# Kernel tuning notes

Hardware: AMD Instinct MI355X
Metric: run time of the kernel (lower is better)

The kernel has to match this reference:

```python
import jax, jax.numpy as jnp
import numpy as np

B, C, H, W = 2, 192, 256, 256
HEADS = 6


def _conv1x1(x, w, b):
    # x: [b,ci,h,w], w: [co,ci,1,1], b: [co]
    return jnp.einsum('oi,bihw->bohw', w[:, :, 0, 0], x) + b[None, :, None, None]


def _dwconv3x3(x, w, b):
    # depthwise 3x3, padding=1; x: [b,c,h,w], w: [c,1,3,3], b: [c]
    y = jax.lax.conv_general_dilated(
        x, w, window_strides=(1, 1), padding='SAME',
        feature_group_count=x.shape[1],
        dimension_numbers=('NCHW', 'OIHW', 'NCHW'))
    return y + b[None, :, None, None]


def _l2norm(t, eps=1e-12):
    # F.normalize(dim=-1): x / max(||x||_2, eps)
    n = jnp.sqrt(jnp.sum(t * t, axis=-1, keepdims=True))
    return t / jnp.maximum(n, eps)


def setup_inputs() -> dict:
    key = jax.random.key(0)
    ks = jax.random.split(key, 12)
    s = 0.02
    return {
        'feat_guide': jax.random.normal(ks[0], (B, C, H, W), jnp.float32),
        'feat_op': jax.random.normal(ks[1], (B, C, H, W), jnp.float32),
        'q_w': jax.random.normal(ks[2], (C, C, 1, 1), jnp.float32) * s,
        'q_b': jax.random.normal(ks[3], (C,), jnp.float32) * s,
        'kv_w': jax.random.normal(ks[4], (2 * C, C, 1, 1), jnp.float32) * s,
        'kv_b': jax.random.normal(ks[5], (2 * C,), jnp.float32) * s,
        'q_dw_w': jax.random.normal(ks[6], (C, 1, 3, 3), jnp.float32) * s,
        'q_dw_b': jax.random.normal(ks[7], (C,), jnp.float32) * s,
        'kv_dw_w': jax.random.normal(ks[8], (2 * C, 1, 3, 3), jnp.float32) * s,
        'kv_dw_b': jax.random.normal(ks[9], (2 * C,), jnp.float32) * s,
        'proj_w': jax.random.normal(ks[10], (C, C, 1, 1), jnp.float32) * s,
        'proj_b': jax.random.normal(ks[11], (C,), jnp.float32) * s,
        'temperature': jnp.ones((HEADS, 1, 1), jnp.float32),
    }


def reference(feat_guide, feat_op, q_w, q_b, kv_w, kv_b, q_dw_w, q_dw_b,
              kv_dw_w, kv_dw_b, proj_w, proj_b, temperature):
    b, c, h, w = feat_guide.shape
    q = _dwconv3x3(_conv1x1(feat_guide, q_w, q_b), q_dw_w, q_dw_b)
    kv = _dwconv3x3(_conv1x1(feat_op, kv_w, kv_b), kv_dw_w, kv_dw_b)
    k, v = jnp.split(kv, 2, axis=1)

    def heads(t):  # [b,c,h,w] -> [b,heads,c/heads,hw]
        return t.reshape(b, HEADS, c // HEADS, h * w)

    q = _l2norm(heads(q))
    k = _l2norm(heads(k))
    v = heads(v)
    # channel-wise attention: [b,heads,c',c'] scores over hw
    attn = jnp.einsum('bhcn,bhdn->bhcd', q, k) * temperature[None]
    attn = jax.nn.softmax(attn, axis=-1)
    out = jnp.einsum('bhcd,bhdn->bhcn', attn, v).reshape(b, c, h, w)
    return _conv1x1(out, proj_w, proj_b)
```

## Files before the change

kernel.cpp:

```cpp
#include <hip/hip_runtime.h>

#define HW_N 65536
#define CC 192
#define NCHUNKS 128

typedef __attribute__((ext_vector_type(8))) short short8v;
typedef __attribute__((ext_vector_type(4))) short short4v;
typedef __attribute__((ext_vector_type(4))) float f32x4;

__device__ __forceinline__ float bf2f(unsigned short u) {
  union { unsigned int i; float f; } v; v.i = ((unsigned int)u) << 16; return v.f;
}
__device__ __forceinline__ unsigned short f2bf(float f) {
  union { float f; unsigned int i; } v; v.f = f;
  unsigned int r = v.i + 0x7fffu + ((v.i >> 16) & 1u);
  return (unsigned short)(r >> 16);
}

__global__ __launch_bounds__(256) void cvt_w(
    const float* __restrict__ qw, const float* __restrict__ kvw,
    unsigned short* __restrict__ Wq, unsigned short* __restrict__ Wkv) {
  const int i = (blockIdx.x * 256 + threadIdx.x) * 8;
  const float* src; unsigned short* dst; int off;
  if (i < 36864) { src = qw; dst = Wq; off = i; }
  else { src = kvw; dst = Wkv; off = i - 36864; }
  unsigned short tmp[8];
#pragma unroll
  for (int j = 0; j < 8; ++j) tmp[j] = f2bf(src[off + j]);
  *(short8v*)(dst + off) = *(short8v*)tmp;
}

template <int INF32, int OUTF32, int PERB>
__global__ __launch_bounds__(512) void conv_gemm(
    const void* __restrict__ X_, const unsigned short* __restrict__ W,
    const float* __restrict__ bias, void* __restrict__ out_,
    int Mtot, int msplit) {
  __shared__ unsigned short Bt[2][128][40];
  __shared__ unsigned short Rp[96][144];
  const int d = blockIdx.x;
  int mt, nt;
  if (msplit == 2) { mt = (d >> 3) & 1; nt = (d & 7) | ((d >> 4) << 3); }
  else { mt = 0; nt = d; }
  const int m0 = mt * 192, n0 = nt * 128;
  const int b = blockIdx.z;
  const int t = threadIdx.x;
  const int lane = t & 63, wv = t >> 6;
  const int l15 = lane & 15, lg = lane >> 4;
  const int wm = wv & 3, wn = wv >> 2;
  const int mrow = m0 + wm * 48;
  const int nw = wn * 64;
  const int nq = t & 31;
  const int kp = t >> 5;
  const size_t xb = (size_t)b * CC * (size_t)HW_N + n0 + nq * 4;
  const unsigned short* Wb = W + (PERB ? (size_t)b * Mtot * CC : 0);

  unsigned int pk[4];
  auto gload = [&](int kc) {
    const size_t xo = xb + (size_t)(kc * 32 + kp * 2) * (size_t)HW_N;
    if (INF32) {
      f32x4 v0 = *(const f32x4*)((const float*)X_ + xo);
      f32x4 v1 = *(const f32x4*)((const float*)X_ + xo + HW_N);
#pragma unroll
      for (int j = 0; j < 4; ++j)
        pk[j] = (unsigned int)f2bf(v0[j]) | ((unsigned int)f2bf(v1[j]) << 16);
    } else {
      short4v a0 = *(const short4v*)((const unsigned short*)X_ + xo);
      short4v a1 = *(const short4v*)((const unsigned short*)X_ + xo + HW_N);
#pragma unroll
      for (int j = 0; j < 4; ++j)
        pk[j] = (unsigned int)(unsigned short)a0[j] | ((unsigned int)(unsigned short)a1[j] << 16);
    }
  };
  auto lwrite = [&](int buf) {
#pragma unroll
    for (int j = 0; j < 4; ++j)
      *(unsigned int*)&Bt[buf][nq * 4 + j][kp * 2] = pk[j];
  };

  gload(0);
  lwrite(0);
  __syncthreads();

  f32x4 acc[3][4] = {};
  for (int kc = 0; kc < 6; ++kc) {
    const int buf = kc & 1;
    if (kc < 5) gload(kc + 1);
    short8v af[3], bfr[4];
    const int k0 = kc * 32 + lg * 8;
#pragma unroll
    for (int fr = 0; fr < 3; ++fr)
      af[fr] = *(const short8v*)(Wb + (size_t)(mrow + fr * 16 + l15) * CC + k0);
#pragma unroll
    for (int fc = 0; fc < 4; ++fc)
      bfr[fc] = *(const short8v*)&Bt[buf][nw + fc * 16 + l15][lg * 8];
#pragma unroll
    for (int fr = 0; fr < 3; ++fr)
#pragma unroll
      for (int fc = 0; fc < 4; ++fc)
        acc[fr][fc] = __builtin_amdgcn_mfma_f32_16x16x32_bf16(af[fr], bfr[fc], acc[fr][fc], 0, 0, 0);
    if (kc < 5) lwrite(buf ^ 1);
    __syncthreads();
  }

  const size_t obase = (size_t)b * Mtot * (size_t)HW_N;
#pragma unroll
  for (int half = 0; half < 2; ++half) {
    if ((wm >> 1) == half) {
      const int mbase = (wm & 1) * 48;
#pragma unroll
      for (int fr = 0; fr < 3; ++fr) {
#pragma unroll
        for (int r = 0; r < 4; ++r) {
          const int mloc = mbase + fr * 16 + lg * 4 + r;
          const float bb = bias[m0 + half * 96 + mloc];
#pragma unroll
          for (int fc = 0; fc < 4; ++fc)
            Rp[mloc][nw + fc * 16 + l15] = f2bf(acc[fr][fc][r] + bb);
        }
      }
    }
    __syncthreads();
#pragma unroll
    for (int s = 0; s < 3; ++s) {
      const int idx = s * 512 + t;
      const int m = idx >> 4, n8 = (idx & 15) * 8;
      short8v v = *(short8v*)&Rp[m][n8];
      const size_t oo = obase + (size_t)(m0 + half * 96 + m) * HW_N + n0 + n8;
      if (OUTF32) {
        float tmp[8];
#pragma unroll
        for (int j = 0; j < 8; ++j) tmp[j] = bf2f((unsigned short)v[j]);
        *(f32x4*)((float*)out_ + oo) = *(f32x4*)&tmp[0];
        *(f32x4*)((float*)out_ + oo + 4) = *(f32x4*)&tmp[4];
      } else {
        *(short8v*)((unsigned short*)out_ + oo) = v;
      }
    }
    __syncthreads();
  }
}

__global__ __launch_bounds__(256) void dwconv3x3_all(
    const unsigned short* __restrict__ QC, const unsigned short* __restrict__ KVC,
    const float* __restrict__ q_dw_w, const float* __restrict__ q_dw_b,
    const float* __restrict__ kv_dw_w, const float* __restrict__ kv_dw_b,
    unsigned short* __restrict__ Qb, unsigned short* __restrict__ Kb,
    unsigned short* __restrict__ Vb) {
  const int t = threadIdx.x;
  const int wc = (t & 31) * 8;
  const int h = blockIdx.x * 8 + (t >> 5);
  const int y = blockIdx.y, b = blockIdx.z;
  const unsigned short* in; const float* w; float bv; unsigned short* out;
  if (y < 192) {
    in = QC + ((size_t)b * 192 + y) * (size_t)HW_N;
    w = q_dw_w + y * 9; bv = q_dw_b[y];
    out = Qb + ((size_t)b * 192 + y) * (size_t)HW_N;
  } else if (y < 384) {
    const int c = y - 192;
    in = KVC + ((size_t)b * 384 + c) * (size_t)HW_N;
    w = kv_dw_w + c * 9; bv = kv_dw_b[c];
    out = Kb + ((size_t)b * 192 + c) * (size_t)HW_N;
  } else {
    const int c = y - 384;
    in = KVC + ((size_t)b * 384 + 192 + c) * (size_t)HW_N;
    w = kv_dw_w + (192 + c) * 9; bv = kv_dw_b[192 + c];
    out = Vb + ((size_t)b * 192 + c) * (size_t)HW_N;
  }
  float wv9[9];
#pragma unroll
  for (int i = 0; i < 9; ++i) wv9[i] = w[i];
  float f[3][10];
#pragma unroll
  for (int ky = 0; ky < 3; ++ky) {
    const int hh = h + ky - 1;
    if (hh < 0 || hh > 255) {
#pragma unroll
      for (int j = 0; j < 10; ++j) f[ky][j] = 0.f;
    } else {
      const unsigned short* row = in + hh * 256;
      short8v v = *(const short8v*)(row + wc);
      f[ky][0] = (wc > 0) ? bf2f(row[wc - 1]) : 0.f;
#pragma unroll
      for (int j = 0; j < 8; ++j) f[ky][1 + j] = bf2f((unsigned short)v[j]);
      f[ky][9] = (wc < 248) ? bf2f(row[wc + 8]) : 0.f;
    }
  }
  union { short8v v; unsigned short u[8]; } o;
#pragma unroll
  for (int j = 0; j < 8; ++j) {
    float acc = bv;
#pragma unroll
    for (int ky = 0; ky < 3; ++ky)
#pragma unroll
      for (int kx = 0; kx < 3; ++kx)
        acc += wv9[ky * 3 + kx] * f[ky][j + kx];
    o.u[j] = f2bf(acc);
  }
  *(short8v*)(out + h * 256 + wc) = o.v;
}

__global__ __launch_bounds__(64) void gram_kernel(
    const unsigned short* __restrict__ Q, const unsigned short* __restrict__ K,
    float* __restrict__ Gp, float* __restrict__ nqp, float* __restrict__ nkp) {
  const int lane = threadIdx.x;
  const int l15 = lane & 15, lg = lane >> 4;
  const int chunk = blockIdx.x, h = blockIdx.y, b = blockIdx.z;
  const int bh = b * 6 + h;
  const size_t base = ((size_t)b * CC + h * 32) * (size_t)HW_N;
  f32x4 acc[2][2] = {};
  float sq[2] = {0.f, 0.f}, sk[2] = {0.f, 0.f};
  const int nst = chunk * 512 + lg * 8;
  for (int ks = 0; ks < 16; ++ks) {
    const int n = nst + ks * 32;
    short8v qa[2], kb[2];
#pragma unroll
    for (int fr = 0; fr < 2; ++fr) {
      qa[fr] = *(const short8v*)(Q + base + (size_t)(fr * 16 + l15) * HW_N + n);
      kb[fr] = *(const short8v*)(K + base + (size_t)(fr * 16 + l15) * HW_N + n);
    }
#pragma unroll
    for (int fr = 0; fr < 2; ++fr)
#pragma unroll
      for (int j = 0; j < 8; ++j) {
        float a = bf2f((unsigned short)qa[fr][j]); sq[fr] += a * a;
        float c2 = bf2f((unsigned short)kb[fr][j]); sk[fr] += c2 * c2;
      }
#pragma unroll
    for (int fr = 0; fr < 2; ++fr)
#pragma unroll
      for (int fc = 0; fc < 2; ++fc)
        acc[fr][fc] = __builtin_amdgcn_mfma_f32_16x16x32_bf16(qa[fr], kb[fc], acc[fr][fc], 0, 0, 0);
  }
  float* Gb = Gp + (size_t)(chunk * 12 + bh) * 1024;
#pragma unroll
  for (int fr = 0; fr < 2; ++fr)
#pragma unroll
    for (int fc = 0; fc < 2; ++fc)
#pragma unroll
      for (int r = 0; r < 4; ++r)
        Gb[(fr * 16 + lg * 4 + r) * 32 + fc * 16 + l15] = acc[fr][fc][r];
#pragma unroll
  for (int fr = 0; fr < 2; ++fr) {
    float v = sq[fr]; v += __shfl_down(v, 32); v += __shfl_down(v, 16);
    float u = sk[fr]; u += __shfl_down(u, 32); u += __shfl_down(u, 16);
    if (lane < 16) {
      nqp[(size_t)(chunk * 12 + bh) * 32 + fr * 16 + lane] = v;
      nkp[(size_t)(chunk * 12 + bh) * 32 + fr * 16 + lane] = u;
    }
  }
}

__global__ __launch_bounds__(256) void reduce_gram(
    const float* __restrict__ Gp, const float* __restrict__ nqp, const float* __restrict__ nkp,
    float* __restrict__ G, float* __restrict__ nq, float* __restrict__ nk) {
  const int i = blockIdx.x * 256 + threadIdx.x;
  if (i < 12 * 1024) {
    float s = 0.f;
    for (int ch = 0; ch < NCHUNKS; ++ch) s += Gp[(size_t)ch * 12288 + i];
    G[i] = s;
  } else if (i < 12 * 1024 + 384) {
    const int j = i - 12 * 1024;
    float s = 0.f;
    for (int ch = 0; ch < NCHUNKS; ++ch) s += nqp[(size_t)ch * 384 + j];
    nq[j] = s;
  } else if (i < 12 * 1024 + 768) {
    const int j = i - 12 * 1024 - 384;
    float s = 0.f;
    for (int ch = 0; ch < NCHUNKS; ++ch) s += nkp[(size_t)ch * 384 + j];
    nk[j] = s;
  }
}

__global__ __launch_bounds__(256) void attn_proj(
    const float* __restrict__ G, const float* __restrict__ nq, const float* __restrict__ nk,
    const float* __restrict__ temp, const float* __restrict__ proj_w,
    unsigned short* __restrict__ Mout) {
  const int h = blockIdx.x, b = blockIdx.y;
  const int bh = b * 6 + h;
  const int t = threadIdx.x;
  __shared__ float sc[32][33];
  __shared__ float nrmq[32], nrmk[32];
  if (t < 32) nrmq[t] = fmaxf(sqrtf(nq[bh * 32 + t]), 1e-12f);
  else if (t < 64) nrmk[t - 32] = fmaxf(sqrtf(nk[bh * 32 + t - 32]), 1e-12f);
  __syncthreads();
  const float tpr = temp[h];
  for (int i = t; i < 1024; i += 256) {
    const int c = i >> 5, d = i & 31;
    sc[c][d] = G[bh * 1024 + i] * tpr / (nrmq[c] * nrmk[d]);
  }
  __syncthreads();
  if (t < 32) {
    float mx = -1e30f;
    for (int d = 0; d < 32; ++d) mx = fmaxf(mx, sc[t][d]);
    float sum = 0.f;
    for (int d = 0; d < 32; ++d) { float e = __expf(sc[t][d] - mx); sc[t][d] = e; sum += e; }
    const float inv = 1.f / sum;
    for (int d = 0; d < 32; ++d) sc[t][d] *= inv;
  }
  __syncthreads();
  for (int i = t; i < 6144; i += 256) {
    const int co = i >> 5, d = i & 31;
    float acc = 0.f;
    for (int c = 0; c < 32; ++c) acc += proj_w[co * CC + h * 32 + c] * sc[c][d];
    Mout[((size_t)b * CC + co) * CC + h * 32 + d] = f2bf(acc);
  }
}

extern "C" void kernel_launch(void* const* d_in, const int* in_sizes, int n_in,
                              void* d_out, int out_size, void* d_ws, size_t ws_size,
                              hipStream_t stream) {
  const float* fg = (const float*)d_in[0];
  const float* fo = (const float*)d_in[1];
  const float* q_w = (const float*)d_in[2];
  const float* q_b = (const float*)d_in[3];
  const float* kv_w = (const float*)d_in[4];
  const float* kv_b = (const float*)d_in[5];
  const float* q_dw_w = (const float*)d_in[6];
  const float* q_dw_b = (const float*)d_in[7];
  const float* kv_dw_w = (const float*)d_in[8];
  const float* kv_dw_b = (const float*)d_in[9];
  const float* proj_w = (const float*)d_in[10];
  const float* proj_b = (const float*)d_in[11];
  const float* temp = (const float*)d_in[12];

  char* ws = (char*)d_ws;
  unsigned short* QC  = (unsigned short*)(ws + 0);
  unsigned short* KVC = (unsigned short*)(ws + 50331648);
  unsigned short* Qb  = (unsigned short*)(ws + 150994944);
  unsigned short* Kb  = (unsigned short*)(ws + 0);
  unsigned short* Vb  = (unsigned short*)(ws + 50331648);
  float* Gp  = (float*)(ws + 201326592);
  float* nqp = (float*)(ws + 207618048);
  float* nkp = (float*)(ws + 207814656);
  float* G   = (float*)(ws + 208011264);
  float* nqv = (float*)(ws + 208060416);
  float* nkv = (float*)(ws + 208061952);
  unsigned short* Mw  = (unsigned short*)(ws + 208063488);
  unsigned short* Wq  = (unsigned short*)(ws + 208210944);
  unsigned short* Wkv = (unsigned short*)(ws + 208284672);

  cvt_w<<<dim3(54), dim3(256), 0, stream>>>(q_w, kv_w, Wq, Wkv);
  conv_gemm<1, 0, 0><<<dim3(512, 1, 2), dim3(512), 0, stream>>>(
      (const void*)fg, Wq, q_b, (void*)QC, 192, 1);
  conv_gemm<1, 0, 0><<<dim3(1024, 1, 2), dim3(512), 0, stream>>>(
      (const void*)fo, Wkv, kv_b, (void*)KVC, 384, 2);
  dwconv3x3_all<<<dim3(32, 576, 2), dim3(256), 0, stream>>>(
      QC, KVC, q_dw_w, q_dw_b, kv_dw_w, kv_dw_b, Qb, Kb, Vb);
  gram_kernel<<<dim3(NCHUNKS, 6, 2), dim3(64), 0, stream>>>(Qb, Kb, Gp, nqp, nkp);
  reduce_gram<<<dim3(51), dim3(256), 0, stream>>>(Gp, nqp, nkp, G, nqv, nkv);
  attn_proj<<<dim3(6, 2), dim3(256), 0, stream>>>(G, nqv, nkv, temp, proj_w, Mw);
  conv_gemm<0, 1, 1><<<dim3(512, 1, 2), dim3(512), 0, stream>>>(
      (const void*)Vb, Mw, proj_b, d_out, 192, 1);
}
```

Measured before the change: 300.4 us.

## Preload GEMM weight fragments, swizzle LDS tile, compute two rows per dwconv thread

The conv GEMM now loads all six k-steps of A-operand weight fragments into registers up front instead of reloading them from global memory each iteration. The kc loop is fully unrolled. The B tile in LDS uses an XOR swizzle on write and read to cut bank conflicts. The depthwise 3x3 kernel now gives each thread two output rows, so the three input rows are shared across outputs and the grid is halved. The cost is higher register pressure: 18 short8v weight fragments per thread in the GEMM and more live floats in the dwconv, which could lower occupancy.

```diff
diff --git a/kernel.cpp b/kernel.cpp
--- a/kernel.cpp
+++ b/kernel.cpp
@@ -54,6 +54,13 @@
   const size_t xb = (size_t)b * CC * (size_t)HW_N + n0 + nq * 4;
   const unsigned short* Wb = W + (PERB ? (size_t)b * Mtot * CC : 0);
 
+  short8v af[6][3];
+#pragma unroll
+  for (int ks = 0; ks < 6; ++ks)
+#pragma unroll
+    for (int fr = 0; fr < 3; ++fr)
+      af[ks][fr] = *(const short8v*)(Wb + (size_t)(mrow + fr * 16 + l15) * CC + ks * 32 + lg * 8);
+
   unsigned int pk[4];
   auto gload = [&](int kc) {
     const size_t xo = xb + (size_t)(kc * 32 + kp * 2) * (size_t)HW_N;
@@ -71,10 +78,11 @@
         pk[j] = (unsigned int)(unsigned short)a0[j] | ((unsigned int)(unsigned short)a1[j] << 16);
     }
   };
+  const int oswz = ((kp >> 2) ^ (nq & 3)) * 8 + (kp & 3) * 2;
   auto lwrite = [&](int buf) {
 #pragma unroll
     for (int j = 0; j < 4; ++j)
-      *(unsigned int*)&Bt[buf][nq * 4 + j][kp * 2] = pk[j];
+      *(unsigned int*)&Bt[buf][nq * 4 + j][oswz] = pk[j];
   };
 
   gload(0);
@@ -82,22 +90,21 @@
   __syncthreads();
 
   f32x4 acc[3][4] = {};
+#pragma unroll
   for (int kc = 0; kc < 6; ++kc) {
     const int buf = kc & 1;
     if (kc < 5) gload(kc + 1);
-    short8v af[3], bfr[4];
-    const int k0 = kc * 32 + lg * 8;
+    short8v bfr[4];
+#pragma unroll
+    for (int fc = 0; fc < 4; ++fc) {
+      const int nn = nw + fc * 16 + l15;
+      bfr[fc] = *(const short8v*)&Bt[buf][nn][(lg ^ ((nn >> 2) & 3)) * 8];
+    }
 #pragma unroll
     for (int fr = 0; fr < 3; ++fr)
-      af[fr] = *(const short8v*)(Wb + (size_t)(mrow + fr * 16 + l15) * CC + k0);
-#pragma unroll
-    for (int fc = 0; fc < 4; ++fc)
-      bfr[fc] = *(const short8v*)&Bt[buf][nw + fc * 16 + l15][lg * 8];
-#pragma unroll
-    for (int fr = 0; fr < 3; ++fr)
 #pragma unroll
       for (int fc = 0; fc < 4; ++fc)
-        acc[fr][fc] = __builtin_amdgcn_mfma_f32_16x16x32_bf16(af[fr], bfr[fc], acc[fr][fc], 0, 0, 0);
+        acc[fr][fc] = __builtin_amdgcn_mfma_f32_16x16x32_bf16(af[kc][fr], bfr[fc], acc[fr][fc], 0, 0, 0);
     if (kc < 5) lwrite(buf ^ 1);
     __syncthreads();
   }
@@ -148,7 +155,7 @@
     unsigned short* __restrict__ Vb) {
   const int t = threadIdx.x;
   const int wc = (t & 31) * 8;
-  const int h = blockIdx.x * 8 + (t >> 5);
+  const int h0 = blockIdx.x * 16 + (t >> 5) * 2;
   const int y = blockIdx.y, b = blockIdx.z;
   const unsigned short* in; const float* w; float bv; unsigned short* out;
   if (y < 192) {
@@ -169,10 +176,10 @@
   float wv9[9];
 #pragma unroll
   for (int i = 0; i < 9; ++i) wv9[i] = w[i];
-  float f[3][10];
-#pragma unroll
-  for (int ky = 0; ky < 3; ++ky) {
-    const int hh = h + ky - 1;
+  float f[4][10];
+#pragma unroll
+  for (int ky = 0; ky < 4; ++ky) {
+    const int hh = h0 + ky - 1;
     if (hh < 0 || hh > 255) {
 #pragma unroll
       for (int j = 0; j < 10; ++j) f[ky][j] = 0.f;
@@ -185,18 +192,21 @@
       f[ky][9] = (wc < 248) ? bf2f(row[wc + 8]) : 0.f;
     }
   }
-  union { short8v v; unsigned short u[8]; } o;
-#pragma unroll
-  for (int j = 0; j < 8; ++j) {
-    float acc = bv;
-#pragma unroll
-    for (int ky = 0; ky < 3; ++ky)
-#pragma unroll
-      for (int kx = 0; kx < 3; ++kx)
-        acc += wv9[ky * 3 + kx] * f[ky][j + kx];
-    o.u[j] = f2bf(acc);
-  }
-  *(short8v*)(out + h * 256 + wc) = o.v;
+#pragma unroll
+  for (int rr = 0; rr < 2; ++rr) {
+    union { short8v v; unsigned short u[8]; } o;
+#pragma unroll
+    for (int j = 0; j < 8; ++j) {
+      float acc = bv;
+#pragma unroll
+      for (int ky = 0; ky < 3; ++ky)
+#pragma unroll
+        for (int kx = 0; kx < 3; ++kx)
+          acc += wv9[ky * 3 + kx] * f[rr + ky][j + kx];
+      o.u[j] = f2bf(acc);
+    }
+    *(short8v*)(out + (h0 + rr) * 256 + wc) = o.v;
+  }
 }
 
 __global__ __launch_bounds__(64) void gram_kernel(
@@ -344,7 +354,7 @@
       (const void*)fg, Wq, q_b, (void*)QC, 192, 1);
   conv_gemm<1, 0, 0><<<dim3(1024, 1, 2), dim3(512), 0, stream>>>(
       (const void*)fo, Wkv, kv_b, (void*)KVC, 384, 2);
-  dwconv3x3_all<<<dim3(32, 576, 2), dim3(256), 0, stream>>>(
+  dwconv3x3_all<<<dim3(16, 576, 2), dim3(256), 0, stream>>>(
       QC, KVC, q_dw_w, q_dw_b, kv_dw_w, kv_dw_b, Qb, Kb, Vb);
   gram_kernel<<<dim3(NCHUNKS, 6, 2), dim3(64), 0, stream>>>(Qb, Kb, Gp, nqp, nkp);
   reduce_gram<<<dim3(51), dim3(256), 0, stream>>>(Gp, nqp, nkp, G, nqv, nkv);
```

After: 341.3 us. 1.14x slower.
